# Kernel tuning notes

Hardware: AMD Instinct MI355X
Metric: run time of the kernel (lower is better)

The kernel has to match this reference:

```python
import jax, jax.numpy as jnp
import numpy as np

C = 1.0  # Poincare ball curvature
EPS = 4e-3       # float32 boundary epsilon (hgcn convention)
MIN_NORM = 1e-15


def _norm(x):
    return jnp.maximum(jnp.linalg.norm(x, axis=-1, keepdims=True), MIN_NORM)


def proj(x, c=C):
    # clip points to the open ball of radius (1-eps)/sqrt(c)
    maxnorm = (1.0 - EPS) / jnp.sqrt(c)
    n = _norm(x)
    return jnp.where(n > maxnorm, x / n * maxnorm, x)


def logmap0(x, c=C):
    sqrt_c = jnp.sqrt(c)
    n = _norm(x)
    arg = jnp.clip(sqrt_c * n, -1.0 + 1e-7, 1.0 - 1e-7)
    return x / n * jnp.arctanh(arg) / sqrt_c


def expmap0(u, c=C):
    sqrt_c = jnp.sqrt(c)
    n = _norm(u)
    return jnp.tanh(sqrt_c * n) * u / (sqrt_c * n)


def setup_inputs() -> dict:
    key = jax.random.key(0)
    k1, k2 = jax.random.split(key)
    N, D_IN, D_OUT = 8192, 4096, 4096
    # points inside the unit ball: small-scale gaussian (norm ~ 0.01*sqrt(4096) ~ 0.64)
    x = jax.random.normal(k1, (N, D_IN), dtype=jnp.float32) * 0.01
    # xavier_uniform with gain=sqrt(2)
    bound = np.sqrt(2.0) * np.sqrt(6.0 / (D_IN + D_OUT))
    W = jax.random.uniform(k2, (D_OUT, D_IN), dtype=jnp.float32, minval=-bound, maxval=bound)
    b = jnp.zeros((D_OUT,), dtype=jnp.float32)
    return {"x": x, "W": W, "b": b}


def reference(x, W, b):
    # CustomHyperbolicLinear (euc_tangent_fc path, activation=Identity):
    # logmap0 -> dense linear -> expmap0 -> proj
    t = logmap0(x)
    t = t @ W.T + b
    y = proj(expmap0(t))
    # outer activation: CustomHyperbolicActivation(Tanh)
    # proj -> logmap0 -> tanh -> proj_tan0 (identity on Poincare) -> expmap0 -> proj
    y = proj(y)
    t2 = jnp.tanh(logmap0(y))
    out = proj(expmap0(t2))
    return out
```

## Files before the change

kernel.cpp:

```cpp
#include <hip/hip_runtime.h>
#include <stdint.h>
#include <math.h>

#define GM 8192
#define GN 4096
#define GK 4096
#define BM 128
#define BN 128
#define BK 32

typedef __bf16 bf16x8 __attribute__((ext_vector_type(8)));
typedef float  f32x4  __attribute__((ext_vector_type(4)));

typedef const __attribute__((address_space(1))) void* gas_ptr;
typedef __attribute__((address_space(3))) void* las_ptr;

__device__ __forceinline__ unsigned short f2bf(float f) {
    union { float f; unsigned u; } a; a.f = f;
    unsigned r = a.u + 0x7FFFu + ((a.u >> 16) & 1u);
    return (unsigned short)(r >> 16);
}
__device__ __forceinline__ float bf2f(unsigned short h) {
    union { unsigned u; float f; } a; a.u = ((unsigned)h) << 16;
    return a.f;
}

__device__ __forceinline__ float fast_tanh(float x) {
    float xc = fminf(fmaxf(x, -15.f), 15.f);
    float e = __expf(2.f * xc);
    return (e - 1.f) * __builtin_amdgcn_rcpf(e + 1.f);
}
__device__ __forceinline__ float fast_atanh(float x) {
    return 0.5f * __logf((1.f + x) * __builtin_amdgcn_rcpf(1.f - x));
}

__global__ __launch_bounds__(256) void pre_kernel(const float* __restrict__ x,
                                                  const float* __restrict__ W,
                                                  unsigned short* __restrict__ t,
                                                  unsigned short* __restrict__ Wb) {
    const int lane = threadIdx.x & 63;
    const int wv   = threadIdx.x >> 6;
    if (blockIdx.x < 2048) {
        const int row = blockIdx.x * 4 + wv;
        const float* xr = x + (size_t)row * GK;
        float v[64];
        float ss = 0.f;
#pragma unroll
        for (int j = 0; j < 16; ++j) {
            f32x4 p = *(const f32x4*)(xr + (size_t)(j * 64 + lane) * 4);
#pragma unroll
            for (int e = 0; e < 4; ++e) { v[j * 4 + e] = p[e]; ss += p[e] * p[e]; }
        }
#pragma unroll
        for (int off = 32; off; off >>= 1) ss += __shfl_xor(ss, off);
        const float n = fmaxf(sqrtf(ss), 1e-15f);
        const float scale = fast_atanh(fminf(n, 1.f - 1e-7f)) * __builtin_amdgcn_rcpf(n);
        unsigned short* tr = t + (size_t)row * GK;
#pragma unroll
        for (int j = 0; j < 16; ++j) {
            ushort4 o;
            o.x = f2bf(v[j * 4 + 0] * scale);
            o.y = f2bf(v[j * 4 + 1] * scale);
            o.z = f2bf(v[j * 4 + 2] * scale);
            o.w = f2bf(v[j * 4 + 3] * scale);
            *(ushort4*)(tr + (size_t)(j * 64 + lane) * 4) = o;
        }
    } else {
        const int row = (blockIdx.x - 2048) * 4 + wv;
        const float* wr = W + (size_t)row * GK;
        unsigned short* wo = Wb + (size_t)row * GK;
#pragma unroll 4
        for (int j = 0; j < 16; ++j) {
            f32x4 p = *(const f32x4*)(wr + (size_t)(j * 64 + lane) * 4);
            ushort4 o;
            o.x = f2bf(p[0]); o.y = f2bf(p[1]); o.z = f2bf(p[2]); o.w = f2bf(p[3]);
            *(ushort4*)(wo + (size_t)(j * 64 + lane) * 4) = o;
        }
    }
}

template <bool BF16C>
__global__ __launch_bounds__(256, 4) void gemm_kernel(const unsigned short* __restrict__ A,
                                                      const unsigned short* __restrict__ B,
                                                      void* __restrict__ Cv) {
    __shared__ __align__(16) unsigned short lA[BM * BK];
    __shared__ __align__(16) unsigned short lB[BN * BK];

    const int tid  = threadIdx.x;
    const int wave = tid >> 6;
    const int lane = tid & 63;
    const int m16  = lane & 15;
    const int quad = lane >> 4;
    const int waveM = (wave >> 1) * 64;
    const int waveN = (wave & 1) * 64;
    const int tileM = blockIdx.y * BM;
    const int tileN = blockIdx.x * BN;

    const int rA = lane >> 2;
    const int kg = (lane & 3) * 8;

    const unsigned short* aPtr = A + (size_t)(tileM + wave * 32 + rA) * GK + kg;
    const unsigned short* bPtr = B + (size_t)(tileN + wave * 32 + rA) * GK + kg;
    las_ptr ldsA = (las_ptr)&lA[wave * 1024];
    las_ptr ldsB = (las_ptr)&lB[wave * 1024];

    f32x4 acc[4][4] = {};

#pragma unroll 1
    for (int k0 = 0; k0 < GK; k0 += BK) {
        __builtin_amdgcn_global_load_lds((gas_ptr)(aPtr + k0),                   ldsA, 16, 0, 0);
        __builtin_amdgcn_global_load_lds((gas_ptr)(aPtr + k0 + (size_t)16 * GK), (las_ptr)((char*)ldsA + 1024), 16, 0, 0);
        __builtin_amdgcn_global_load_lds((gas_ptr)(bPtr + k0),                   ldsB, 16, 0, 0);
        __builtin_amdgcn_global_load_lds((gas_ptr)(bPtr + k0 + (size_t)16 * GK), (las_ptr)((char*)ldsB + 1024), 16, 0, 0);
        __syncthreads();

        bf16x8 af[4], bfr[4];
#pragma unroll
        for (int i = 0; i < 4; ++i) {
            af[i]  = *(const bf16x8*)&lA[(waveM + i * 16 + m16) * BK + quad * 8];
            bfr[i] = *(const bf16x8*)&lB[(waveN + i * 16 + m16) * BK + quad * 8];
        }
#pragma unroll
        for (int mi = 0; mi < 4; ++mi)
#pragma unroll
            for (int ni = 0; ni < 4; ++ni)
                acc[mi][ni] = __builtin_amdgcn_mfma_f32_16x16x32_bf16(af[mi], bfr[ni], acc[mi][ni], 0, 0, 0);
        __syncthreads();
    }

#pragma unroll
    for (int mi = 0; mi < 4; ++mi)
#pragma unroll
        for (int ni = 0; ni < 4; ++ni)
#pragma unroll
            for (int r = 0; r < 4; ++r) {
                const int row = tileM + waveM + mi * 16 + quad * 4 + r;
                const int col = tileN + waveN + ni * 16 + m16;
                if (BF16C)
                    ((unsigned short*)Cv)[(size_t)row * GN + col] = f2bf(acc[mi][ni][r]);
                else
                    ((float*)Cv)[(size_t)row * GN + col] = acc[mi][ni][r];
            }
}

template <bool BF16C>
__global__ __launch_bounds__(256) void epilogue_kernel(const void* __restrict__ Cv,
                                                       const float* __restrict__ bias,
                                                       float* __restrict__ out) {
    const int lane = threadIdx.x & 63;
    const int row  = blockIdx.x * 4 + (threadIdx.x >> 6);
    float u[64];
    float ss = 0.f;
#pragma unroll
    for (int j = 0; j < 16; ++j) {
        const size_t col = (size_t)(j * 64 + lane) * 4;
        f32x4 bb = *(const f32x4*)(bias + col);
        if (BF16C) {
            ushort4 p = *(const ushort4*)((const unsigned short*)Cv + (size_t)row * GN + col);
            float q0 = bf2f(p.x) + bb[0], q1 = bf2f(p.y) + bb[1];
            float q2 = bf2f(p.z) + bb[2], q3 = bf2f(p.w) + bb[3];
            u[j * 4 + 0] = q0; u[j * 4 + 1] = q1; u[j * 4 + 2] = q2; u[j * 4 + 3] = q3;
            ss += q0 * q0 + q1 * q1 + q2 * q2 + q3 * q3;
        } else {
            f32x4 p = *(const f32x4*)((const float*)Cv + (size_t)row * GN + col);
#pragma unroll
            for (int e = 0; e < 4; ++e) { float q = p[e] + bb[e]; u[j * 4 + e] = q; ss += q * q; }
        }
    }
#pragma unroll
    for (int off = 32; off; off >>= 1) ss += __shfl_xor(ss, off);

    const float n1 = fmaxf(sqrtf(ss), 1e-15f);
    const float ny = fminf(fast_tanh(n1), 0.996f);
    const float g = (ny * __builtin_amdgcn_rcpf(n1)) *
                    (fast_atanh(ny) * __builtin_amdgcn_rcpf(fmaxf(ny, 1e-15f)));

    float ss2 = 0.f;
#pragma unroll
    for (int i = 0; i < 64; ++i) { float q = fast_tanh(u[i] * g); u[i] = q; ss2 += q * q; }
#pragma unroll
    for (int off = 32; off; off >>= 1) ss2 += __shfl_xor(ss2, off);

    const float n3 = fmaxf(sqrtf(ss2), 1e-15f);
    const float s3 = fminf(fast_tanh(n3), 0.996f) * __builtin_amdgcn_rcpf(n3);
    float* orow = out + (size_t)row * GN;
#pragma unroll
    for (int j = 0; j < 16; ++j) {
        f32x4 o;
#pragma unroll
        for (int e = 0; e < 4; ++e) o[e] = u[j * 4 + e] * s3;
        *(f32x4*)(orow + (size_t)(j * 64 + lane) * 4) = o;
    }
}

extern "C" void kernel_launch(void* const* d_in, const int* in_sizes, int n_in,
                              void* d_out, int out_size, void* d_ws, size_t ws_size,
                              hipStream_t stream) {
    const float* x = (const float*)d_in[0];
    const float* W = (const float*)d_in[1];
    const float* b = (const float*)d_in[2];
    float* out = (float*)d_out;

    unsigned short* t_bf = (unsigned short*)d_ws;
    unsigned short* W_bf = t_bf + (size_t)GM * GK;
    unsigned short* C_bf = W_bf + (size_t)GN * GK;
    const size_t need_bf16c = ((size_t)GM * GK + (size_t)GN * GK + (size_t)GM * GN) * 2;
    const bool bf16c = ws_size >= need_bf16c;

    pre_kernel<<<2048 + 1024, 256, 0, stream>>>(x, W, t_bf, W_bf);
    if (bf16c) {
        gemm_kernel<true><<<dim3(GN / BN, GM / BM), 256, 0, stream>>>(t_bf, W_bf, (void*)C_bf);
        epilogue_kernel<true><<<2048, 256, 0, stream>>>((const void*)C_bf, b, out);
    } else {
        gemm_kernel<false><<<dim3(GN / BN, GM / BM), 256, 0, stream>>>(t_bf, W_bf, (void*)out);
        epilogue_kernel<false><<<2048, 256, 0, stream>>>((const void*)out, b, out);
    }
}
```

Baseline: 601.1 us.

## Rewrite GEMM with 256x256 tiles, double-buffered swizzled LDS and pipelined loads

Replaces the 128x128x32 single-buffer GEMM with a 256x256x64 tile kernel using 512 threads, a 128KB double-buffered LDS with XOR swizzle, and global-to-LDS prefetch of the next k-steps interleaved with MFMA phases. It also remaps block IDs to group tiles for L2 locality and raises wave priority around MFMA bursts. The aim is to hide global-load latency behind compute, raise arithmetic intensity per tile and remove LDS bank conflicts. The cost is more registers and LDS per block, which limits occupancy, plus fragile hand-placed waitcnt and barrier ordering.

```diff
diff --git a/kernel.cpp b/kernel.cpp
--- a/kernel.cpp
+++ b/kernel.cpp
@@ -5,9 +5,11 @@
 #define GM 8192
 #define GN 4096
 #define GK 4096
-#define BM 128
-#define BN 128
-#define BK 32
+
+#define BM 256
+#define BN 256
+#define BK 64
+#define NT (GK / BK)
 
 typedef __bf16 bf16x8 __attribute__((ext_vector_type(8)));
 typedef float  f32x4  __attribute__((ext_vector_type(4)));
@@ -80,56 +82,139 @@
 }
 
 template <bool BF16C>
-__global__ __launch_bounds__(256, 4) void gemm_kernel(const unsigned short* __restrict__ A,
+__global__ __launch_bounds__(512, 2) void gemm_kernel(const unsigned short* __restrict__ A,
                                                       const unsigned short* __restrict__ B,
                                                       void* __restrict__ Cv) {
-    __shared__ __align__(16) unsigned short lA[BM * BK];
-    __shared__ __align__(16) unsigned short lB[BN * BK];
+    __shared__ __align__(16) unsigned short lds[65536];
 
     const int tid  = threadIdx.x;
-    const int wave = tid >> 6;
+    const int w    = tid >> 6;
     const int lane = tid & 63;
     const int m16  = lane & 15;
     const int quad = lane >> 4;
-    const int waveM = (wave >> 1) * 64;
-    const int waveN = (wave & 1) * 64;
-    const int tileM = blockIdx.y * BM;
-    const int tileN = blockIdx.x * BN;
-
-    const int rA = lane >> 2;
-    const int kg = (lane & 3) * 8;
-
-    const unsigned short* aPtr = A + (size_t)(tileM + wave * 32 + rA) * GK + kg;
-    const unsigned short* bPtr = B + (size_t)(tileN + wave * 32 + rA) * GK + kg;
-    las_ptr ldsA = (las_ptr)&lA[wave * 1024];
-    las_ptr ldsB = (las_ptr)&lB[wave * 1024];
-
-    f32x4 acc[4][4] = {};
-
-#pragma unroll 1
-    for (int k0 = 0; k0 < GK; k0 += BK) {
-        __builtin_amdgcn_global_load_lds((gas_ptr)(aPtr + k0),                   ldsA, 16, 0, 0);
-        __builtin_amdgcn_global_load_lds((gas_ptr)(aPtr + k0 + (size_t)16 * GK), (las_ptr)((char*)ldsA + 1024), 16, 0, 0);
-        __builtin_amdgcn_global_load_lds((gas_ptr)(bPtr + k0),                   ldsB, 16, 0, 0);
-        __builtin_amdgcn_global_load_lds((gas_ptr)(bPtr + k0 + (size_t)16 * GK), (las_ptr)((char*)ldsB + 1024), 16, 0, 0);
-        __syncthreads();
-
-        bf16x8 af[4], bfr[4];
-#pragma unroll
-        for (int i = 0; i < 4; ++i) {
-            af[i]  = *(const bf16x8*)&lA[(waveM + i * 16 + m16) * BK + quad * 8];
-            bfr[i] = *(const bf16x8*)&lB[(waveN + i * 16 + m16) * BK + quad * 8];
-        }
-#pragma unroll
-        for (int mi = 0; mi < 4; ++mi)
-#pragma unroll
-            for (int ni = 0; ni < 4; ++ni)
-                acc[mi][ni] = __builtin_amdgcn_mfma_f32_16x16x32_bf16(af[mi], bfr[ni], acc[mi][ni], 0, 0, 0);
-        __syncthreads();
-    }
-
-#pragma unroll
-    for (int mi = 0; mi < 4; ++mi)
+
+    const int bid = blockIdx.x;
+    const int wid = (bid & 7) * 64 + (bid >> 3);
+    const int tileM = (wid >> 4) * BM;
+    const int tileN = (wid & 15) * BN;
+
+    const int waveM = (w >> 2) * 128;
+    const int waveN = (w & 3) * 64;
+
+    const int rS   = w * 16 + (lane >> 2);
+    const int swzS = (rS >> 1) & 3;
+    const int colS = ((lane & 3) ^ swzS) * 8;
+    const unsigned short* a0 = A + (size_t)(tileM + rS) * GK + colS;
+    const unsigned short* a1 = a0 + (size_t)128 * GK;
+    const unsigned short* b0 = B + (size_t)(tileN + rS) * GK + colS;
+    const unsigned short* b1 = b0 + (size_t)128 * GK;
+
+#define STAGE(DBUF, MAT, KH, KEL)                                                                      \
+    do {                                                                                               \
+        const int _off = (DBUF) * 65536 + (MAT) * 32768 + (KH) * 16384 + w * 1024;                     \
+        const unsigned short* _s0 = ((MAT) ? b0 : a0) + (KEL) + (KH) * 32;                             \
+        const unsigned short* _s1 = ((MAT) ? b1 : a1) + (KEL) + (KH) * 32;                             \
+        __builtin_amdgcn_global_load_lds((gas_ptr)_s0, (las_ptr)((char*)lds + _off), 16, 0, 0);        \
+        __builtin_amdgcn_global_load_lds((gas_ptr)_s1, (las_ptr)((char*)lds + _off + 8192), 16, 0, 0); \
+    } while (0)
+
+    int aoff[8], boff[4];
+#pragma unroll
+    for (int mi = 0; mi < 8; ++mi) {
+        const int r = waveM + mi * 16 + m16;
+        aoff[mi] = r * 64 + ((quad ^ ((r >> 1) & 3)) << 4);
+    }
+#pragma unroll
+    for (int ni = 0; ni < 4; ++ni) {
+        const int r = waveN + ni * 16 + m16;
+        boff[ni] = r * 64 + ((quad ^ ((r >> 1) & 3)) << 4);
+    }
+
+#define FRAG(OFF) (*(const bf16x8*)((const char*)lds + (OFF)))
+
+#define MFMA_BLOCK(MBASE)                                                            \
+    {                                                                                \
+        _Pragma("unroll")                                                            \
+        for (int mi = 0; mi < 4; ++mi) {                                             \
+            _Pragma("unroll")                                                        \
+            for (int ni = 0; ni < 4; ++ni)                                           \
+                acc[(MBASE) + mi][ni] = __builtin_amdgcn_mfma_f32_16x16x32_bf16(     \
+                    af[mi], bf[ni], acc[(MBASE) + mi][ni], 0, 0, 0);                 \
+        }                                                                            \
+    }
+
+    f32x4 acc[8][4] = {};
+    bf16x8 af[4], bf[4];
+
+    STAGE(0, 0, 0, 0);
+    STAGE(0, 1, 0, 0);
+    STAGE(0, 0, 1, 0);
+    STAGE(0, 1, 1, 0);
+    STAGE(1, 0, 0, BK);
+    STAGE(1, 1, 0, BK);
+    asm volatile("s_waitcnt vmcnt(8)" ::: "memory");
+    __builtin_amdgcn_s_barrier();
+
+#pragma unroll 2
+    for (int t = 0; t < NT; ++t) {
+        const int b  = t & 1;
+        const int bn = b ^ 1;
+        const int abase0 = b * 65536;
+        const int abase1 = abase0 + 16384;
+        const int bbase0 = abase0 + 32768;
+        const int bbase1 = bbase0 + 16384;
+        const int k1 = (t + 1 < NT ? t + 1 : NT - 1) * BK;
+        const int k2 = (t + 2 < NT ? t + 2 : NT - 1) * BK;
+
+        af[0] = FRAG(abase0 + aoff[0]); af[1] = FRAG(abase0 + aoff[1]);
+        af[2] = FRAG(abase0 + aoff[2]); af[3] = FRAG(abase0 + aoff[3]);
+        bf[0] = FRAG(bbase0 + boff[0]); bf[1] = FRAG(bbase0 + boff[1]);
+        bf[2] = FRAG(bbase0 + boff[2]); bf[3] = FRAG(bbase0 + boff[3]);
+        STAGE(bn, 0, 1, k1);
+        __builtin_amdgcn_s_barrier();
+        asm volatile("s_waitcnt lgkmcnt(0)" ::: "memory");
+        __builtin_amdgcn_s_setprio(1);
+        MFMA_BLOCK(0);
+        __builtin_amdgcn_s_setprio(0);
+        __builtin_amdgcn_s_barrier();
+
+        af[0] = FRAG(abase0 + aoff[4]); af[1] = FRAG(abase0 + aoff[5]);
+        af[2] = FRAG(abase0 + aoff[6]); af[3] = FRAG(abase0 + aoff[7]);
+        STAGE(bn, 1, 1, k1);
+        __builtin_amdgcn_s_barrier();
+        asm volatile("s_waitcnt lgkmcnt(0)" ::: "memory");
+        __builtin_amdgcn_s_setprio(1);
+        MFMA_BLOCK(4);
+        __builtin_amdgcn_s_setprio(0);
+        asm volatile("s_waitcnt vmcnt(8)" ::: "memory");
+        __builtin_amdgcn_s_barrier();
+
+        af[0] = FRAG(abase1 + aoff[0]); af[1] = FRAG(abase1 + aoff[1]);
+        af[2] = FRAG(abase1 + aoff[2]); af[3] = FRAG(abase1 + aoff[3]);
+        bf[0] = FRAG(bbase1 + boff[0]); bf[1] = FRAG(bbase1 + boff[1]);
+        bf[2] = FRAG(bbase1 + boff[2]); bf[3] = FRAG(bbase1 + boff[3]);
+        STAGE(b, 0, 0, k2);
+        __builtin_amdgcn_s_barrier();
+        asm volatile("s_waitcnt lgkmcnt(0)" ::: "memory");
+        __builtin_amdgcn_s_setprio(1);
+        MFMA_BLOCK(0);
+        __builtin_amdgcn_s_setprio(0);
+        __builtin_amdgcn_s_barrier();
+
+        af[0] = FRAG(abase1 + aoff[4]); af[1] = FRAG(abase1 + aoff[5]);
+        af[2] = FRAG(abase1 + aoff[6]); af[3] = FRAG(abase1 + aoff[7]);
+        STAGE(b, 1, 0, k2);
+        __builtin_amdgcn_s_barrier();
+        asm volatile("s_waitcnt lgkmcnt(0)" ::: "memory");
+        __builtin_amdgcn_s_setprio(1);
+        MFMA_BLOCK(4);
+        __builtin_amdgcn_s_setprio(0);
+        asm volatile("s_waitcnt vmcnt(8)" ::: "memory");
+        __builtin_amdgcn_s_barrier();
+    }
+
+#pragma unroll
+    for (int mi = 0; mi < 8; ++mi)
 #pragma unroll
         for (int ni = 0; ni < 4; ++ni)
 #pragma unroll
@@ -141,6 +226,9 @@
                 else
                     ((float*)Cv)[(size_t)row * GN + col] = acc[mi][ni][r];
             }
+#undef STAGE
+#undef FRAG
+#undef MFMA_BLOCK
 }
 
 template <bool BF16C>
@@ -208,11 +296,12 @@
     const bool bf16c = ws_size >= need_bf16c;
 
     pre_kernel<<<2048 + 1024, 256, 0, stream>>>(x, W, t_bf, W_bf);
+    const int nwg = (GM / BM) * (GN / BN);
     if (bf16c) {
-        gemm_kernel<true><<<dim3(GN / BN, GM / BM), 256, 0, stream>>>(t_bf, W_bf, (void*)C_bf);
+        gemm_kernel<true><<<nwg, 512, 0, stream>>>(t_bf, W_bf, (void*)C_bf);
         epilogue_kernel<true><<<2048, 256, 0, stream>>>((const void*)C_bf, b, out);
     } else {
-        gemm_kernel<false><<<dim3(GN / BN, GM / BM), 256, 0, stream>>>(t_bf, W_bf, (void*)out);
+        gemm_kernel<false><<<nwg, 512, 0, stream>>>(t_bf, W_bf, (void*)out);
         epilogue_kernel<false><<<2048, 256, 0, stream>>>((const void*)out, b, out);
     }
 }
```

New measurement: 531.6 us. -11.6%, faster.
